# Performance work log

Hardware: AMD Instinct MI355X
Metric: run time of the kernel (lower is better)

## Reference

```python
import jax, jax.numpy as jnp
import numpy as np

B, H, W, C = 2, 64, 64, 192
DM = int(2.0 * C)   # d_inner = ssm_ratio * hidden_dim = 384
N = 16              # d_state
R = 12              # dt_rank = ceil(C / 16)
K = 4               # scan directions


def _ln(x, g, b, eps):
    mu = jnp.mean(x, axis=-1, keepdims=True)
    var = jnp.var(x, axis=-1, keepdims=True)
    return (x - mu) * jax.lax.rsqrt(var + eps) * g + b


def setup_inputs() -> dict:
    key = jax.random.key(0)
    ks = jax.random.split(key, 8)
    return {
        "input": jax.random.normal(ks[0], (B, H, W, C), jnp.float32),
        "norm_g": jnp.ones((C,), jnp.float32),
        "norm_b": jnp.zeros((C,), jnp.float32),
        "in_proj_w": jax.random.normal(ks[1], (C, 2 * DM), jnp.float32) * 0.02,
        "conv_w": jax.random.normal(ks[2], (DM, 1, 3, 3), jnp.float32) * 0.1,
        "conv_b": jnp.zeros((DM,), jnp.float32),
        "x_proj_w": jax.random.normal(ks[3], (K, R + 2 * N, DM), jnp.float32) * 0.02,
        "dt_w": jax.random.normal(ks[4], (K, DM, R), jnp.float32) * 0.1,
        "dt_b": jax.random.uniform(ks[5], (K, DM), jnp.float32, -4.0, -2.0),
        "A_logs": jnp.tile(jnp.log(jnp.arange(1, N + 1, dtype=jnp.float32))[None, None, :], (K, DM, 1)),
        "Ds": jnp.ones((K, DM), jnp.float32),
        "out_norm_g": jnp.ones((DM,), jnp.float32),
        "out_norm_b": jnp.zeros((DM,), jnp.float32),
        "out_proj_w": jax.random.normal(ks[6], (DM, C), jnp.float32) * 0.02,
    }


def _selective_scan(us, deltas, A, Bs, Cs):
    # us, deltas: (B,K,D,L); A: (K,D,N); Bs, Cs: (B,K,N,L)
    u_l = jnp.moveaxis(us, -1, 0)       # (L,B,K,D)
    d_l = jnp.moveaxis(deltas, -1, 0)   # (L,B,K,D)
    B_l = jnp.moveaxis(Bs, -1, 0)       # (L,B,K,N)
    C_l = jnp.moveaxis(Cs, -1, 0)       # (L,B,K,N)
    h0 = jnp.zeros(us.shape[:3] + (A.shape[-1],), us.dtype)  # (B,K,D,N)

    def step(h, xs):
        u_t, d_t, b_t, c_t = xs
        dA = jnp.exp(d_t[..., None] * A)                       # (B,K,D,N)
        h = dA * h + (d_t * u_t)[..., None] * b_t[:, :, None, :]
        y = jnp.einsum('bkdn,bkn->bkd', h, c_t)
        return h, y

    _, ys = jax.lax.scan(step, h0, (u_l, d_l, B_l, C_l))
    return jnp.moveaxis(ys, 0, -1)  # (B,K,D,L)


def reference(input, norm_g, norm_b, in_proj_w, conv_w, conv_b, x_proj_w,
              dt_w, dt_b, A_logs, Ds, out_norm_g, out_norm_b, out_proj_w):
    Bz, Hh, Ww, Cc = input.shape
    L = Hh * Ww
    # pre-norm
    xn = _ln(input, norm_g, norm_b, 1e-6)
    # input projection -> x, z
    xz = xn @ in_proj_w                      # (B,H,W,2*DM)
    x, z = jnp.split(xz, 2, axis=-1)
    # depthwise conv + SiLU (channels-first)
    x = jnp.transpose(x, (0, 3, 1, 2))       # (B,DM,H,W)
    Dm = x.shape[1]
    x = jax.lax.conv_general_dilated(
        x, conv_w, (1, 1), 'SAME',
        dimension_numbers=('NCHW', 'OIHW', 'NCHW'),
        feature_group_count=Dm) + conv_b[None, :, None, None]
    x = jax.nn.silu(x)
    # 4-direction cross-scan: hw, wh, and their reverses
    x_flat = x.reshape(Bz, Dm, L)
    x_t = jnp.transpose(x, (0, 1, 3, 2)).reshape(Bz, Dm, L)
    xs = jnp.stack([x_flat, x_t], axis=1)                  # (B,2,DM,L)
    xs = jnp.concatenate([xs, jnp.flip(xs, -1)], axis=1)   # (B,4,DM,L)
    Rr = dt_w.shape[2]
    Nn = A_logs.shape[2]
    x_dbl = jnp.einsum('bkdl,kcd->bkcl', xs, x_proj_w)     # (B,4,R+2N,L)
    dts, Bs, Cs = jnp.split(x_dbl, [Rr, Rr + Nn], axis=2)
    deltas = jax.nn.softplus(
        jnp.einsum('bkrl,kdr->bkdl', dts, dt_w) + dt_b[None, :, :, None])
    A = -jnp.exp(A_logs)                                   # (4,DM,N)
    out_y = _selective_scan(xs, deltas, A, Bs, Cs) + Ds[None, :, :, None] * xs
    # merge the 4 directions back
    inv = jnp.flip(out_y[:, 2:], -1)

    def wh(t):
        return jnp.transpose(t.reshape(Bz, Dm, Ww, Hh), (0, 1, 3, 2)).reshape(Bz, Dm, L)

    y = out_y[:, 0] + inv[:, 0] + wh(out_y[:, 1]) + wh(inv[:, 1])  # (B,DM,L)
    y = jnp.transpose(y, (0, 2, 1))                                # (B,L,DM)
    y = _ln(y, out_norm_g, out_norm_b, 1e-5).reshape(Bz, Hh, Ww, Dm)
    y = y * jax.nn.silu(z)
    out = y @ out_proj_w
    # residual (drop_path=0 -> identity)
    return input + out
```

## Files before the change

kernel.cpp:

```cpp
#include <hip/hip_runtime.h>
#include <hip/hip_bf16.h>


typedef __attribute__((ext_vector_type(8))) short short8;
typedef __attribute__((ext_vector_type(4))) float floatx4;

__global__ __launch_bounds__(256) void k_ln(const float* __restrict__ in,
                                            const float* __restrict__ g,
                                            const float* __restrict__ be,
                                            __hip_bfloat16* __restrict__ out) {
  int row = blockIdx.x * 4 + (threadIdx.x >> 6);
  int lane = threadIdx.x & 63;
  const float* x = in + (long)row * 192;
  float v0 = x[lane], v1 = x[lane + 64], v2 = x[lane + 128];
  float s = v0 + v1 + v2;
  float s2 = v0 * v0 + v1 * v1 + v2 * v2;
  #pragma unroll
  for (int o = 32; o > 0; o >>= 1) { s += __shfl_xor(s, o); s2 += __shfl_xor(s2, o); }
  float mu = s * (1.f / 192.f);
  float var = s2 * (1.f / 192.f) - mu * mu;
  float r = rsqrtf(var + 1e-6f);
  __hip_bfloat16* op = out + (long)row * 192;
  op[lane]       = __float2bfloat16((v0 - mu) * r * g[lane]       + be[lane]);
  op[lane + 64]  = __float2bfloat16((v1 - mu) * r * g[lane + 64]  + be[lane + 64]);
  op[lane + 128] = __float2bfloat16((v2 - mu) * r * g[lane + 128] + be[lane + 128]);
}

__global__ __launch_bounds__(256) void k_packw(const float* __restrict__ ipw,
                                               const float* __restrict__ xpw,
                                               const float* __restrict__ opw,
                                               __hip_bfloat16* __restrict__ Wt1,
                                               __hip_bfloat16* __restrict__ Wt2,
                                               __hip_bfloat16* __restrict__ Wt3) {
  int idx = blockIdx.x * 256 + threadIdx.x;
  if (idx < 147456) {
    int n = idx / 192, k = idx - n * 192;
    Wt1[idx] = __float2bfloat16(ipw[(long)k * 768 + n]);
  } else if (idx < 147456 + 73728) {
    int t = idx - 147456;
    int j = t / 384;
    float v = (j < 176) ? xpw[t] : 0.f;
    Wt2[t] = __float2bfloat16(v);
  } else if (idx < 147456 + 73728 + 73728) {
    int t = idx - 147456 - 73728;
    int n = t / 384, k = t - n * 384;
    Wt3[t] = __float2bfloat16(opw[(long)k * 192 + n]);
  }
}

__device__ __forceinline__ int inv_dir(int k, int p) {
  int pt = ((p & 63) << 6) | (p >> 6);
  if (k == 0) return p;
  if (k == 1) return pt;
  if (k == 2) return 4095 - p;
  return 4095 - pt;
}
__device__ __forceinline__ int dir_pix(int k, int l) { return inv_dir(k, l); }

template <int EPI>
__global__ __launch_bounds__(256) void k_gemm_mfma(const __hip_bfloat16* __restrict__ A,
                                                   const __hip_bfloat16* __restrict__ Bt,
                                                   const float* __restrict__ Res,
                                                   float* __restrict__ Co,
                                                   __hip_bfloat16* __restrict__ CoB,
                                                   __hip_bfloat16* __restrict__ Co2B,
                                                   float* __restrict__ dtsS,
                                                   float* __restrict__ BsS,
                                                   float* __restrict__ CsS,
                                                   int M, int N, int Kk) {
  __shared__ __align__(16) short As[64 * 64];
  __shared__ __align__(16) short Bs[64 * 64];
  int tid = threadIdx.x;
  int wave = tid >> 6, lane = tid & 63;
  int mlane = lane & 15, quad = lane >> 4;
  int row0 = blockIdx.y * 64, col0 = blockIdx.x * 64;
  int wr = wave & 1, wc = wave >> 1;
  floatx4 acc[2][2];
  #pragma unroll
  for (int mi = 0; mi < 2; mi++)
    #pragma unroll
    for (int ni = 0; ni < 2; ni++) acc[mi][ni] = (floatx4){0.f, 0.f, 0.f, 0.f};

  for (int k0 = 0; k0 < Kk; k0 += 64) {
    #pragma unroll
    for (int c = tid; c < 512; c += 256) {
      int r = c >> 3, j = c & 7;
      *(float4*)&As[r * 64 + ((j ^ (r & 7)) << 3)] =
          *(const float4*)&A[(long)(row0 + r) * Kk + k0 + j * 8];
    }
    #pragma unroll
    for (int c = tid; c < 512; c += 256) {
      int r = c >> 3, j = c & 7;
      *(float4*)&Bs[r * 64 + ((j ^ (r & 7)) << 3)] =
          *(const float4*)&Bt[(long)(col0 + r) * Kk + k0 + j * 8];
    }
    __syncthreads();
    short8 af[2][2], bf[2][2];
    #pragma unroll
    for (int mi = 0; mi < 2; mi++) {
      int r = wr * 32 + mi * 16 + mlane;
      #pragma unroll
      for (int kk = 0; kk < 2; kk++) {
        int jx = (kk * 4 + quad) ^ (r & 7);
        af[mi][kk] = *(const short8*)&As[r * 64 + jx * 8];
      }
    }
    #pragma unroll
    for (int ni = 0; ni < 2; ni++) {
      int rn = wc * 32 + ni * 16 + mlane;
      #pragma unroll
      for (int kk = 0; kk < 2; kk++) {
        int jx = (kk * 4 + quad) ^ (rn & 7);
        bf[ni][kk] = *(const short8*)&Bs[rn * 64 + jx * 8];
      }
    }
    #pragma unroll
    for (int kk = 0; kk < 2; kk++)
      #pragma unroll
      for (int mi = 0; mi < 2; mi++)
        #pragma unroll
        for (int ni = 0; ni < 2; ni++)
          acc[mi][ni] = __builtin_amdgcn_mfma_f32_16x16x32_bf16(af[mi][kk], bf[ni][kk],
                                                                acc[mi][ni], 0, 0, 0);
    __syncthreads();
  }
  #pragma unroll
  for (int mi = 0; mi < 2; mi++) {
    #pragma unroll
    for (int ni = 0; ni < 2; ni++) {
      int cc = col0 + wc * 32 + ni * 16 + mlane;
      #pragma unroll
      for (int i = 0; i < 4; i++) {
        int rr = row0 + wr * 32 + mi * 16 + quad * 4 + i;
        float v = acc[mi][ni][i];
        if (EPI == 1) {
          Co[(long)rr * N + cc] = v + Res[(long)rr * N + cc];
        } else if (EPI == 2) {
          if (cc < 384) CoB[(long)rr * 384 + cc] = __float2bfloat16(v);
          else          Co2B[(long)rr * 384 + (cc - 384)] = __float2bfloat16(v);
        } else {
          if (cc < 176) {
            int k4 = (cc >= 132) ? 3 : (cc >= 88) ? 2 : (cc >= 44) ? 1 : 0;
            int c = cc - k4 * 44;
            int b = rr >> 12, p = rr & 4095;
            int l = inv_dir(k4, p);
            long lbase = ((long)((b << 2) + k4) << 12) + l;
            if (c < 12)      dtsS[lbase * 12 + c] = v;
            else if (c < 28) BsS[lbase * 16 + (c - 12)] = v;
            else             CsS[lbase * 16 + (c - 28)] = v;
          }
        }
      }
    }
  }
}

__global__ __launch_bounds__(384) void k_conv(const __hip_bfloat16* __restrict__ xbufB,
                                              const float* __restrict__ cw,
                                              const float* __restrict__ cb,
                                              __hip_bfloat16* __restrict__ xcb) {
  int row = blockIdx.x;
  int b = row >> 12, p = row & 4095;
  int h = p >> 6, w0 = p & 63;
  int d = threadIdx.x;
  float acc = cb[d];
  const float* wt = cw + d * 9;
  #pragma unroll
  for (int dh = -1; dh <= 1; dh++) {
    int hh = h + dh;
    if (hh < 0 || hh > 63) continue;
    #pragma unroll
    for (int dw = -1; dw <= 1; dw++) {
      int ww = w0 + dw;
      if (ww < 0 || ww > 63) continue;
      acc += __bfloat162float(xbufB[((long)(b << 12) + (hh << 6) + ww) * 384 + d])
             * wt[(dh + 1) * 3 + (dw + 1)];
    }
  }
  float sg = 1.f / (1.f + __expf(-acc));
  xcb[(long)row * 384 + d] = __float2bfloat16(acc * sg);
}

__device__ __forceinline__ void pow16(float r, float* pws) {
  pws[0] = r;
  #pragma unroll
  for (int n = 1; n < 16; n++) {
    int m = n + 1, c = (m + 1) / 2, f = m - c;
    pws[n] = pws[c - 1] * pws[f - 1];
  }
}

__global__ __launch_bounds__(384) void k_scan0(
    const float* __restrict__ dtsS, const float* __restrict__ BsS,
    const __hip_bfloat16* __restrict__ xcb,
    const float* __restrict__ A_logs, const float* __restrict__ dt_w,
    const float* __restrict__ dt_b,
    float* __restrict__ Eb, float* __restrict__ Dend) {
  int bid = blockIdx.x;
  int s = bid & 127, bk = bid >> 7;
  int k = bk & 3, b = bk >> 2;
  int d = threadIdx.x;
  float w[12];
  const float* dwp = dt_w + ((long)(k * 384) + d) * 12;
  #pragma unroll
  for (int r = 0; r < 12; r++) w[r] = dwp[r];
  float db = dt_b[k * 384 + d];
  const float* al = A_logs + ((long)(k * 384) + d) * 16;
  bool pw = true;
  float av[16];
  #pragma unroll
  for (int n = 0; n < 16; n++) {
    float a = __expf(al[n]);
    av[n] = -a;
    pw = pw && (fabsf(a - (float)(n + 1)) < 1e-3f);
  }
  float h[16];
  #pragma unroll
  for (int n = 0; n < 16; n++) h[n] = 0.f;
  float cum = 0.f;
  long lb = (long)bk * 4096 + s * 32;
  long bpix = (long)(b << 12);

  if (pw) {
    #pragma unroll 4
    for (int t = 0; t < 32; t++) {
      const float4* dq = (const float4*)(dtsS + (lb + t) * 12);
      float4 q0 = dq[0], q1 = dq[1], q2 = dq[2];
      float x = db + q0.x * w[0] + q0.y * w[1] + q0.z * w[2] + q0.w * w[3]
                   + q1.x * w[4] + q1.y * w[5] + q1.z * w[6] + q1.w * w[7]
                   + q2.x * w[8] + q2.y * w[9] + q2.z * w[10] + q2.w * w[11];
      float e = __expf(x);
      float delta = (x > 15.f) ? x : __logf(1.f + e);
      cum += delta;
      int p = dir_pix(k, s * 32 + t);
      float u = __bfloat162float(xcb[(bpix + p) * 384 + d]);
      float du = delta * u;
      float rr = __builtin_amdgcn_rcpf(1.f + e);
      float pws[16]; pow16(rr, pws);
      const float4* Bq = (const float4*)(BsS + (lb + t) * 16);
      float4 b0 = Bq[0], b1 = Bq[1], b2 = Bq[2], b3 = Bq[3];
      float Bl[16] = {b0.x, b0.y, b0.z, b0.w, b1.x, b1.y, b1.z, b1.w,
                      b2.x, b2.y, b2.z, b2.w, b3.x, b3.y, b3.z, b3.w};
      #pragma unroll
      for (int n = 0; n < 16; n++) h[n] = pws[n] * h[n] + du * Bl[n];
    }
  } else {
    for (int t = 0; t < 32; t++) {
      const float4* dq = (const float4*)(dtsS + (lb + t) * 12);
      float4 q0 = dq[0], q1 = dq[1], q2 = dq[2];
      float x = db + q0.x * w[0] + q0.y * w[1] + q0.z * w[2] + q0.w * w[3]
                   + q1.x * w[4] + q1.y * w[5] + q1.z * w[6] + q1.w * w[7]
                   + q2.x * w[8] + q2.y * w[9] + q2.z * w[10] + q2.w * w[11];
      float e = __expf(x);
      float delta = (x > 15.f) ? x : __logf(1.f + e);
      cum += delta;
      int p = dir_pix(k, s * 32 + t);
      float u = __bfloat162float(xcb[(bpix + p) * 384 + d]);
      float du = delta * u;
      const float4* Bq = (const float4*)(BsS + (lb + t) * 16);
      float4 b0 = Bq[0], b1 = Bq[1], b2 = Bq[2], b3 = Bq[3];
      float Bl[16] = {b0.x, b0.y, b0.z, b0.w, b1.x, b1.y, b1.z, b1.w,
                      b2.x, b2.y, b2.z, b2.w, b3.x, b3.y, b3.z, b3.w};
      #pragma unroll
      for (int n = 0; n < 16; n++) {
        float dA = __expf(delta * av[n]);
        h[n] = dA * h[n] + du * Bl[n];
      }
    }
  }
  long g = (long)bk * 128 + s;
  float* Ep = Eb + g * 6144 + d * 16;
  #pragma unroll
  for (int n = 0; n < 16; n++) Ep[n] = h[n];
  Dend[g * 384 + d] = cum;
}

__global__ __launch_bounds__(256) void k_combine(float* __restrict__ Eb,
                                                 const float* __restrict__ Dend,
                                                 const float* __restrict__ A_logs) {
  int t = blockIdx.x * 256 + threadIdx.x;
  int bk = t / 6144;
  int dn = t - bk * 6144;
  int k = bk & 3;
  int d = dn >> 4;
  float av = -__expf(A_logs[(long)k * 6144 + dn]);
  float h = 0.f;
  long ebase = (long)bk * 128 * 6144 + dn;
  long dbase = (long)bk * 128 * 384 + d;
  for (int s = 0; s < 128; s++) {
    long ei = ebase + (long)s * 6144;
    float e = Eb[ei];
    float cum = Dend[dbase + (long)s * 384];
    Eb[ei] = h;
    h = __expf(av * cum) * h + e;
  }
}

__global__ __launch_bounds__(384) void k_scan1(
    const float* __restrict__ dtsS, const float* __restrict__ BsS,
    const float* __restrict__ CsS, const __hip_bfloat16* __restrict__ xcb,
    const float* __restrict__ A_logs, const float* __restrict__ dt_w,
    const float* __restrict__ dt_b, const float* __restrict__ Eb,
    float* __restrict__ ysum) {
  int bid = blockIdx.x;
  int s = bid & 127, bk = bid >> 7;
  int k = bk & 3, b = bk >> 2;
  int d = threadIdx.x;
  float w[12];
  const float* dwp = dt_w + ((long)(k * 384) + d) * 12;
  #pragma unroll
  for (int r = 0; r < 12; r++) w[r] = dwp[r];
  float db = dt_b[k * 384 + d];
  const float* al = A_logs + ((long)(k * 384) + d) * 16;
  bool pw = true;
  float av[16];
  #pragma unroll
  for (int n = 0; n < 16; n++) {
    float a = __expf(al[n]);
    av[n] = -a;
    pw = pw && (fabsf(a - (float)(n + 1)) < 1e-3f);
  }
  float h[16];
  const float* hp = Eb + ((long)bk * 128 + s) * 6144 + d * 16;
  #pragma unroll
  for (int n = 0; n < 16; n++) h[n] = hp[n];
  long lb = (long)bk * 4096 + s * 32;
  long bpix = (long)(b << 12);

  if (pw) {
    #pragma unroll 4
    for (int t = 0; t < 32; t++) {
      const float4* dq = (const float4*)(dtsS + (lb + t) * 12);
      float4 q0 = dq[0], q1 = dq[1], q2 = dq[2];
      float x = db + q0.x * w[0] + q0.y * w[1] + q0.z * w[2] + q0.w * w[3]
                   + q1.x * w[4] + q1.y * w[5] + q1.z * w[6] + q1.w * w[7]
                   + q2.x * w[8] + q2.y * w[9] + q2.z * w[10] + q2.w * w[11];
      float e = __expf(x);
      float delta = (x > 15.f) ? x : __logf(1.f + e);
      int p = dir_pix(k, s * 32 + t);
      float u = __bfloat162float(xcb[(bpix + p) * 384 + d]);
      float du = delta * u;
      float rr = __builtin_amdgcn_rcpf(1.f + e);
      float pws[16]; pow16(rr, pws);
      const float4* Bq = (const float4*)(BsS + (lb + t) * 16);
      float4 b0 = Bq[0], b1 = Bq[1], b2 = Bq[2], b3 = Bq[3];
      float Bl[16] = {b0.x, b0.y, b0.z, b0.w, b1.x, b1.y, b1.z, b1.w,
                      b2.x, b2.y, b2.z, b2.w, b3.x, b3.y, b3.z, b3.w};
      const float4* Cq = (const float4*)(CsS + (lb + t) * 16);
      float4 c0 = Cq[0], c1 = Cq[1], c2 = Cq[2], c3 = Cq[3];
      float Cl[16] = {c0.x, c0.y, c0.z, c0.w, c1.x, c1.y, c1.z, c1.w,
                      c2.x, c2.y, c2.z, c2.w, c3.x, c3.y, c3.z, c3.w};
      float y = 0.f;
      #pragma unroll
      for (int n = 0; n < 16; n++) { h[n] = pws[n] * h[n] + du * Bl[n]; y += h[n] * Cl[n]; }
      atomicAdd(&ysum[(bpix + p) * 384 + d], y);
    }
  } else {
    for (int t = 0; t < 32; t++) {
      const float4* dq = (const float4*)(dtsS + (lb + t) * 12);
      float4 q0 = dq[0], q1 = dq[1], q2 = dq[2];
      float x = db + q0.x * w[0] + q0.y * w[1] + q0.z * w[2] + q0.w * w[3]
                   + q1.x * w[4] + q1.y * w[5] + q1.z * w[6] + q1.w * w[7]
                   + q2.x * w[8] + q2.y * w[9] + q2.z * w[10] + q2.w * w[11];
      float e = __expf(x);
      float delta = (x > 15.f) ? x : __logf(1.f + e);
      int p = dir_pix(k, s * 32 + t);
      float u = __bfloat162float(xcb[(bpix + p) * 384 + d]);
      float du = delta * u;
      const float4* Bq = (const float4*)(BsS + (lb + t) * 16);
      float4 b0 = Bq[0], b1 = Bq[1], b2 = Bq[2], b3 = Bq[3];
      float Bl[16] = {b0.x, b0.y, b0.z, b0.w, b1.x, b1.y, b1.z, b1.w,
                      b2.x, b2.y, b2.z, b2.w, b3.x, b3.y, b3.z, b3.w};
      const float4* Cq = (const float4*)(CsS + (lb + t) * 16);
      float4 c0 = Cq[0], c1 = Cq[1], c2 = Cq[2], c3 = Cq[3];
      float Cl[16] = {c0.x, c0.y, c0.z, c0.w, c1.x, c1.y, c1.z, c1.w,
                      c2.x, c2.y, c2.z, c2.w, c3.x, c3.y, c3.z, c3.w};
      float y = 0.f;
      #pragma unroll
      for (int n = 0; n < 16; n++) {
        float dA = __expf(delta * av[n]);
        h[n] = dA * h[n] + du * Bl[n];
        y += h[n] * Cl[n];
      }
      atomicAdd(&ysum[(bpix + p) * 384 + d], y);
    }
  }
}

__global__ __launch_bounds__(384) void k_merge(const float* __restrict__ ysum,
                                               const __hip_bfloat16* __restrict__ xcb,
                                               const __hip_bfloat16* __restrict__ zbufB,
                                               const float* __restrict__ Ds,
                                               const float* __restrict__ g,
                                               const float* __restrict__ be,
                                               __hip_bfloat16* __restrict__ yactb) {
  int row = blockIdx.x;
  int d = threadIdx.x;
  float v = ysum[(long)row * 384 + d];
  float sd = Ds[d] + Ds[384 + d] + Ds[768 + d] + Ds[1152 + d];
  v += __bfloat162float(xcb[(long)row * 384 + d]) * sd;
  float s1 = v, s2 = v * v;
  #pragma unroll
  for (int o = 32; o > 0; o >>= 1) { s1 += __shfl_xor(s1, o); s2 += __shfl_xor(s2, o); }
  __shared__ float r1[6], r2[6];
  int wv = threadIdx.x >> 6;
  if ((threadIdx.x & 63) == 0) { r1[wv] = s1; r2[wv] = s2; }
  __syncthreads();
  float S1 = 0.f, S2 = 0.f;
  #pragma unroll
  for (int i = 0; i < 6; i++) { S1 += r1[i]; S2 += r2[i]; }
  float mu = S1 * (1.f / 384.f);
  float var = S2 * (1.f / 384.f) - mu * mu;
  float rr = rsqrtf(var + 1e-5f);
  float yn = (v - mu) * rr * g[d] + be[d];
  float z = __bfloat162float(zbufB[(long)row * 384 + d]);
  float sg = z / (1.f + __expf(-z));
  yactb[(long)row * 384 + d] = __float2bfloat16(yn * sg);
}

extern "C" void kernel_launch(void* const* d_in, const int* in_sizes, int n_in,
                              void* d_out, int out_size, void* d_ws, size_t ws_size,
                              hipStream_t stream) {
  const float* input      = (const float*)d_in[0];
  const float* norm_g     = (const float*)d_in[1];
  const float* norm_b     = (const float*)d_in[2];
  const float* in_proj_w  = (const float*)d_in[3];
  const float* conv_w     = (const float*)d_in[4];
  const float* conv_b     = (const float*)d_in[5];
  const float* x_proj_w   = (const float*)d_in[6];
  const float* dt_w       = (const float*)d_in[7];
  const float* dt_b       = (const float*)d_in[8];
  const float* A_logs     = (const float*)d_in[9];
  const float* Ds         = (const float*)d_in[10];
  const float* out_norm_g = (const float*)d_in[11];
  const float* out_norm_b = (const float*)d_in[12];
  const float* out_proj_w = (const float*)d_in[13];
  float* out = (float*)d_out;

  float* ws = (float*)d_ws;
  long o = 0;
  __hip_bfloat16* xnb   = (__hip_bfloat16*)(ws + o); o += 786432;
  __hip_bfloat16* xbufB = (__hip_bfloat16*)(ws + o); o += 1572864;
  __hip_bfloat16* zbufB = (__hip_bfloat16*)(ws + o); o += 1572864;
  __hip_bfloat16* xcb   = (__hip_bfloat16*)(ws + o); o += 1572864;
  __hip_bfloat16* Wt1   = (__hip_bfloat16*)(ws + o); o += 73728;
  __hip_bfloat16* Wt2   = (__hip_bfloat16*)(ws + o); o += 36864;
  __hip_bfloat16* Wt3   = (__hip_bfloat16*)(ws + o); o += 36864;
  float* dtsS           = ws + o;                    o += 393216;
  float* BsS            = ws + o;                    o += 524288;
  float* CsS            = ws + o;                    o += 524288;
  float* Eb             = ws + o;                    o += 6291456;
  float* Dend           = ws + o;                    o += 393216;
  float* ysum           = ws + o;                    o += 3145728;
  __hip_bfloat16* yactb = (__hip_bfloat16*)(ws + o); o += 1572864;

  k_ln<<<dim3(2048), dim3(256), 0, stream>>>(input, norm_g, norm_b, xnb);
  k_packw<<<dim3(1152), dim3(256), 0, stream>>>(in_proj_w, x_proj_w, out_proj_w, Wt1, Wt2, Wt3);
  k_gemm_mfma<2><<<dim3(12, 128), dim3(256), 0, stream>>>(xnb, Wt1, nullptr, nullptr, xbufB, zbufB,
                                                          nullptr, nullptr, nullptr, 8192, 768, 192);
  k_conv<<<dim3(8192), dim3(384), 0, stream>>>(xbufB, conv_w, conv_b, xcb);
  k_gemm_mfma<3><<<dim3(3, 128), dim3(256), 0, stream>>>(xcb, Wt2, nullptr, nullptr, nullptr, nullptr,
                                                         dtsS, BsS, CsS, 8192, 192, 384);
  k_scan0<<<dim3(1024), dim3(384), 0, stream>>>(dtsS, BsS, xcb, A_logs, dt_w, dt_b, Eb, Dend);
  k_combine<<<dim3(192), dim3(256), 0, stream>>>(Eb, Dend, A_logs);
  hipMemsetAsync(ysum, 0, 3145728 * sizeof(float), stream);
  k_scan1<<<dim3(1024), dim3(384), 0, stream>>>(dtsS, BsS, CsS, xcb, A_logs, dt_w, dt_b, Eb, ysum);
  k_merge<<<dim3(8192), dim3(384), 0, stream>>>(ysum, xcb, zbufB, Ds, out_norm_g, out_norm_b, yactb);
  k_gemm_mfma<1><<<dim3(3, 128), dim3(256), 0, stream>>>(yactb, Wt3, input, out, nullptr, nullptr,
                                                         nullptr, nullptr, nullptr, 8192, 192, 384);
}
```

Before: 270.2 us.

## Pair forward/reverse scan directions in one block and batch atomic accumulation

Fuses LayerNorm with weight packing, and moves the ysum zeroing into k_scan0 in place of a separate memset. The scan kernels now use 192-thread blocks with d split across two blocks. k_combine writes prefixes into a separate Hb buffer with 64-thread blocks. k_scan1 processes a forward direction and its reversed partner on the same pixel chunk, reusing the loaded u values and summing both outputs in registers, so it issues half as many atomics. In exchange it needs many more registers (yreg, ureg, two weight sets), which may reduce occupancy, plus extra workspace for Hb.

```diff
diff --git a/kernel.cpp b/kernel.cpp
--- a/kernel.cpp
+++ b/kernel.cpp
@@ -5,46 +5,48 @@
 typedef __attribute__((ext_vector_type(8))) short short8;
 typedef __attribute__((ext_vector_type(4))) float floatx4;
 
-__global__ __launch_bounds__(256) void k_ln(const float* __restrict__ in,
-                                            const float* __restrict__ g,
-                                            const float* __restrict__ be,
-                                            __hip_bfloat16* __restrict__ out) {
-  int row = blockIdx.x * 4 + (threadIdx.x >> 6);
-  int lane = threadIdx.x & 63;
-  const float* x = in + (long)row * 192;
-  float v0 = x[lane], v1 = x[lane + 64], v2 = x[lane + 128];
-  float s = v0 + v1 + v2;
-  float s2 = v0 * v0 + v1 * v1 + v2 * v2;
-  #pragma unroll
-  for (int o = 32; o > 0; o >>= 1) { s += __shfl_xor(s, o); s2 += __shfl_xor(s2, o); }
-  float mu = s * (1.f / 192.f);
-  float var = s2 * (1.f / 192.f) - mu * mu;
-  float r = rsqrtf(var + 1e-6f);
-  __hip_bfloat16* op = out + (long)row * 192;
-  op[lane]       = __float2bfloat16((v0 - mu) * r * g[lane]       + be[lane]);
-  op[lane + 64]  = __float2bfloat16((v1 - mu) * r * g[lane + 64]  + be[lane + 64]);
-  op[lane + 128] = __float2bfloat16((v2 - mu) * r * g[lane + 128] + be[lane + 128]);
-}
-
-__global__ __launch_bounds__(256) void k_packw(const float* __restrict__ ipw,
-                                               const float* __restrict__ xpw,
-                                               const float* __restrict__ opw,
-                                               __hip_bfloat16* __restrict__ Wt1,
-                                               __hip_bfloat16* __restrict__ Wt2,
-                                               __hip_bfloat16* __restrict__ Wt3) {
-  int idx = blockIdx.x * 256 + threadIdx.x;
-  if (idx < 147456) {
-    int n = idx / 192, k = idx - n * 192;
-    Wt1[idx] = __float2bfloat16(ipw[(long)k * 768 + n]);
-  } else if (idx < 147456 + 73728) {
-    int t = idx - 147456;
-    int j = t / 384;
-    float v = (j < 176) ? xpw[t] : 0.f;
-    Wt2[t] = __float2bfloat16(v);
-  } else if (idx < 147456 + 73728 + 73728) {
-    int t = idx - 147456 - 73728;
-    int n = t / 384, k = t - n * 384;
-    Wt3[t] = __float2bfloat16(opw[(long)k * 192 + n]);
+__global__ __launch_bounds__(256) void k_ln_packw(const float* __restrict__ in,
+                                                  const float* __restrict__ g,
+                                                  const float* __restrict__ be,
+                                                  const float* __restrict__ ipw,
+                                                  const float* __restrict__ xpw,
+                                                  const float* __restrict__ opw,
+                                                  __hip_bfloat16* __restrict__ xnb,
+                                                  __hip_bfloat16* __restrict__ Wt1,
+                                                  __hip_bfloat16* __restrict__ Wt2,
+                                                  __hip_bfloat16* __restrict__ Wt3) {
+  int bid = blockIdx.x;
+  if (bid < 2048) {
+    int row = bid * 4 + (threadIdx.x >> 6);
+    int lane = threadIdx.x & 63;
+    const float* x = in + (long)row * 192;
+    float v0 = x[lane], v1 = x[lane + 64], v2 = x[lane + 128];
+    float s = v0 + v1 + v2;
+    float s2 = v0 * v0 + v1 * v1 + v2 * v2;
+    #pragma unroll
+    for (int o = 32; o > 0; o >>= 1) { s += __shfl_xor(s, o); s2 += __shfl_xor(s2, o); }
+    float mu = s * (1.f / 192.f);
+    float var = s2 * (1.f / 192.f) - mu * mu;
+    float r = rsqrtf(var + 1e-6f);
+    __hip_bfloat16* op = xnb + (long)row * 192;
+    op[lane]       = __float2bfloat16((v0 - mu) * r * g[lane]       + be[lane]);
+    op[lane + 64]  = __float2bfloat16((v1 - mu) * r * g[lane + 64]  + be[lane + 64]);
+    op[lane + 128] = __float2bfloat16((v2 - mu) * r * g[lane + 128] + be[lane + 128]);
+  } else {
+    int idx = (bid - 2048) * 256 + threadIdx.x;
+    if (idx < 147456) {
+      int n = idx / 192, k = idx - n * 192;
+      Wt1[idx] = __float2bfloat16(ipw[(long)k * 768 + n]);
+    } else if (idx < 147456 + 73728) {
+      int t = idx - 147456;
+      int j = t / 384;
+      float v = (j < 176) ? xpw[t] : 0.f;
+      Wt2[t] = __float2bfloat16(v);
+    } else if (idx < 147456 + 73728 + 73728) {
+      int t = idx - 147456 - 73728;
+      int n = t / 384, k = t - n * 384;
+      Wt3[t] = __float2bfloat16(opw[(long)k * 192 + n]);
+    }
   }
 }
 
@@ -190,16 +192,23 @@
   }
 }
 
-__global__ __launch_bounds__(384) void k_scan0(
+__global__ __launch_bounds__(192) void k_scan0(
     const float* __restrict__ dtsS, const float* __restrict__ BsS,
     const __hip_bfloat16* __restrict__ xcb,
     const float* __restrict__ A_logs, const float* __restrict__ dt_w,
     const float* __restrict__ dt_b,
-    float* __restrict__ Eb, float* __restrict__ Dend) {
+    float* __restrict__ Eb, float* __restrict__ Dend,
+    float* __restrict__ ysum) {
   int bid = blockIdx.x;
-  int s = bid & 127, bk = bid >> 7;
+  {
+    float4 z4 = {0.f, 0.f, 0.f, 0.f};
+    float4* zp = (float4*)(ysum + (long)bid * 1536) + threadIdx.x;
+    zp[0] = z4; zp[192] = z4;
+  }
+  int half = bid & 1;
+  int s = (bid >> 1) & 127, bk = bid >> 8;
   int k = bk & 3, b = bk >> 2;
-  int d = threadIdx.x;
+  int d = half * 192 + threadIdx.x;
   float w[12];
   const float* dwp = dt_w + ((long)(k * 384) + d) * 12;
   #pragma unroll
@@ -275,10 +284,11 @@
   Dend[g * 384 + d] = cum;
 }
 
-__global__ __launch_bounds__(256) void k_combine(float* __restrict__ Eb,
-                                                 const float* __restrict__ Dend,
-                                                 const float* __restrict__ A_logs) {
-  int t = blockIdx.x * 256 + threadIdx.x;
+__global__ __launch_bounds__(64) void k_combine(const float* __restrict__ Eb,
+                                                const float* __restrict__ Dend,
+                                                const float* __restrict__ A_logs,
+                                                float* __restrict__ Hb) {
+  int t = blockIdx.x * 64 + threadIdx.x;
   int bk = t / 6144;
   int dn = t - bk * 6144;
   int k = bk & 3;
@@ -288,102 +298,182 @@
   long ebase = (long)bk * 128 * 6144 + dn;
   long dbase = (long)bk * 128 * 384 + d;
   for (int s = 0; s < 128; s++) {
-    long ei = ebase + (long)s * 6144;
-    float e = Eb[ei];
-    float cum = Dend[dbase + (long)s * 384];
-    Eb[ei] = h;
-    h = __expf(av * cum) * h + e;
-  }
-}
-
-__global__ __launch_bounds__(384) void k_scan1(
+    Hb[ebase + (long)s * 6144] = h;
+    h = __expf(av * Dend[dbase + (long)s * 384]) * h + Eb[ebase + (long)s * 6144];
+  }
+}
+
+__global__ __launch_bounds__(192) void k_scan1(
     const float* __restrict__ dtsS, const float* __restrict__ BsS,
     const float* __restrict__ CsS, const __hip_bfloat16* __restrict__ xcb,
     const float* __restrict__ A_logs, const float* __restrict__ dt_w,
-    const float* __restrict__ dt_b, const float* __restrict__ Eb,
+    const float* __restrict__ dt_b, const float* __restrict__ Hb,
     float* __restrict__ ysum) {
   int bid = blockIdx.x;
-  int s = bid & 127, bk = bid >> 7;
-  int k = bk & 3, b = bk >> 2;
-  int d = threadIdx.x;
-  float w[12];
-  const float* dwp = dt_w + ((long)(k * 384) + d) * 12;
-  #pragma unroll
-  for (int r = 0; r < 12; r++) w[r] = dwp[r];
-  float db = dt_b[k * 384 + d];
-  const float* al = A_logs + ((long)(k * 384) + d) * 16;
+  int half = bid & 1;
+  int s = (bid >> 1) & 127;
+  int q = (bid >> 8) & 1;
+  int b = bid >> 9;
+  int cf = b * 4 + q;
+  int cr = cf + 2;
+  int sr = 127 - s;
+  int d = half * 192 + threadIdx.x;
+
+  float wf[12], wr2[12];
+  const float* dwf = dt_w + ((long)(q * 384) + d) * 12;
+  const float* dwr = dt_w + ((long)((q + 2) * 384) + d) * 12;
+  #pragma unroll
+  for (int r = 0; r < 12; r++) { wf[r] = dwf[r]; wr2[r] = dwr[r]; }
+  float dbf = dt_b[q * 384 + d];
+  float dbr = dt_b[(q + 2) * 384 + d];
+  const float* alf = A_logs + ((long)(q * 384) + d) * 16;
+  const float* alr = A_logs + ((long)((q + 2) * 384) + d) * 16;
   bool pw = true;
-  float av[16];
+  float avf[16], avr[16];
   #pragma unroll
   for (int n = 0; n < 16; n++) {
-    float a = __expf(al[n]);
-    av[n] = -a;
-    pw = pw && (fabsf(a - (float)(n + 1)) < 1e-3f);
-  }
+    float a1 = __expf(alf[n]), a2 = __expf(alr[n]);
+    avf[n] = -a1; avr[n] = -a2;
+    pw = pw && (fabsf(a1 - (float)(n + 1)) < 1e-3f) && (fabsf(a2 - (float)(n + 1)) < 1e-3f);
+  }
+  long lbf = (long)cf * 4096 + s * 32;
+  long lbr = (long)cr * 4096 + sr * 32;
+  long bpix = (long)(b << 12);
   float h[16];
-  const float* hp = Eb + ((long)bk * 128 + s) * 6144 + d * 16;
-  #pragma unroll
-  for (int n = 0; n < 16; n++) h[n] = hp[n];
-  long lb = (long)bk * 4096 + s * 32;
-  long bpix = (long)(b << 12);
-
+  float yreg[32], ureg[32];
+
+  {
+    const float* hp = Hb + ((long)cf * 128 + s) * 6144 + d * 16;
+    #pragma unroll
+    for (int n = 0; n < 16; n++) h[n] = hp[n];
+  }
   if (pw) {
-    #pragma unroll 4
+    #pragma unroll
     for (int t = 0; t < 32; t++) {
-      const float4* dq = (const float4*)(dtsS + (lb + t) * 12);
+      const float4* dq = (const float4*)(dtsS + (lbf + t) * 12);
       float4 q0 = dq[0], q1 = dq[1], q2 = dq[2];
-      float x = db + q0.x * w[0] + q0.y * w[1] + q0.z * w[2] + q0.w * w[3]
-                   + q1.x * w[4] + q1.y * w[5] + q1.z * w[6] + q1.w * w[7]
-                   + q2.x * w[8] + q2.y * w[9] + q2.z * w[10] + q2.w * w[11];
+      float x = dbf + q0.x * wf[0] + q0.y * wf[1] + q0.z * wf[2] + q0.w * wf[3]
+                    + q1.x * wf[4] + q1.y * wf[5] + q1.z * wf[6] + q1.w * wf[7]
+                    + q2.x * wf[8] + q2.y * wf[9] + q2.z * wf[10] + q2.w * wf[11];
       float e = __expf(x);
       float delta = (x > 15.f) ? x : __logf(1.f + e);
-      int p = dir_pix(k, s * 32 + t);
+      int p = dir_pix(q, s * 32 + t);
       float u = __bfloat162float(xcb[(bpix + p) * 384 + d]);
+      ureg[t] = u;
       float du = delta * u;
       float rr = __builtin_amdgcn_rcpf(1.f + e);
       float pws[16]; pow16(rr, pws);
-      const float4* Bq = (const float4*)(BsS + (lb + t) * 16);
+      const float4* Bq = (const float4*)(BsS + (lbf + t) * 16);
       float4 b0 = Bq[0], b1 = Bq[1], b2 = Bq[2], b3 = Bq[3];
       float Bl[16] = {b0.x, b0.y, b0.z, b0.w, b1.x, b1.y, b1.z, b1.w,
                       b2.x, b2.y, b2.z, b2.w, b3.x, b3.y, b3.z, b3.w};
-      const float4* Cq = (const float4*)(CsS + (lb + t) * 16);
+      const float4* Cq = (const float4*)(CsS + (lbf + t) * 16);
       float4 c0 = Cq[0], c1 = Cq[1], c2 = Cq[2], c3 = Cq[3];
       float Cl[16] = {c0.x, c0.y, c0.z, c0.w, c1.x, c1.y, c1.z, c1.w,
                       c2.x, c2.y, c2.z, c2.w, c3.x, c3.y, c3.z, c3.w};
       float y = 0.f;
       #pragma unroll
       for (int n = 0; n < 16; n++) { h[n] = pws[n] * h[n] + du * Bl[n]; y += h[n] * Cl[n]; }
-      atomicAdd(&ysum[(bpix + p) * 384 + d], y);
+      yreg[t] = y;
     }
   } else {
+    #pragma unroll
     for (int t = 0; t < 32; t++) {
-      const float4* dq = (const float4*)(dtsS + (lb + t) * 12);
+      const float4* dq = (const float4*)(dtsS + (lbf + t) * 12);
       float4 q0 = dq[0], q1 = dq[1], q2 = dq[2];
-      float x = db + q0.x * w[0] + q0.y * w[1] + q0.z * w[2] + q0.w * w[3]
-                   + q1.x * w[4] + q1.y * w[5] + q1.z * w[6] + q1.w * w[7]
-                   + q2.x * w[8] + q2.y * w[9] + q2.z * w[10] + q2.w * w[11];
+      float x = dbf + q0.x * wf[0] + q0.y * wf[1] + q0.z * wf[2] + q0.w * wf[3]
+                    + q1.x * wf[4] + q1.y * wf[5] + q1.z * wf[6] + q1.w * wf[7]
+                    + q2.x * wf[8] + q2.y * wf[9] + q2.z * wf[10] + q2.w * wf[11];
       float e = __expf(x);
       float delta = (x > 15.f) ? x : __logf(1.f + e);
-      int p = dir_pix(k, s * 32 + t);
+      int p = dir_pix(q, s * 32 + t);
       float u = __bfloat162float(xcb[(bpix + p) * 384 + d]);
+      ureg[t] = u;
       float du = delta * u;
-      const float4* Bq = (const float4*)(BsS + (lb + t) * 16);
+      const float4* Bq = (const float4*)(BsS + (lbf + t) * 16);
       float4 b0 = Bq[0], b1 = Bq[1], b2 = Bq[2], b3 = Bq[3];
       float Bl[16] = {b0.x, b0.y, b0.z, b0.w, b1.x, b1.y, b1.z, b1.w,
                       b2.x, b2.y, b2.z, b2.w, b3.x, b3.y, b3.z, b3.w};
-      const float4* Cq = (const float4*)(CsS + (lb + t) * 16);
+      const float4* Cq = (const float4*)(CsS + (lbf + t) * 16);
       float4 c0 = Cq[0], c1 = Cq[1], c2 = Cq[2], c3 = Cq[3];
       float Cl[16] = {c0.x, c0.y, c0.z, c0.w, c1.x, c1.y, c1.z, c1.w,
                       c2.x, c2.y, c2.z, c2.w, c3.x, c3.y, c3.z, c3.w};
       float y = 0.f;
       #pragma unroll
       for (int n = 0; n < 16; n++) {
-        float dA = __expf(delta * av[n]);
+        float dA = __expf(delta * avf[n]);
         h[n] = dA * h[n] + du * Bl[n];
         y += h[n] * Cl[n];
       }
-      atomicAdd(&ysum[(bpix + p) * 384 + d], y);
-    }
+      yreg[t] = y;
+    }
+  }
+  {
+    const float* hp = Hb + ((long)cr * 128 + sr) * 6144 + d * 16;
+    #pragma unroll
+    for (int n = 0; n < 16; n++) h[n] = hp[n];
+  }
+  if (pw) {
+    #pragma unroll
+    for (int tt = 0; tt < 32; tt++) {
+      const float4* dq = (const float4*)(dtsS + (lbr + tt) * 12);
+      float4 q0 = dq[0], q1 = dq[1], q2 = dq[2];
+      float x = dbr + q0.x * wr2[0] + q0.y * wr2[1] + q0.z * wr2[2] + q0.w * wr2[3]
+                    + q1.x * wr2[4] + q1.y * wr2[5] + q1.z * wr2[6] + q1.w * wr2[7]
+                    + q2.x * wr2[8] + q2.y * wr2[9] + q2.z * wr2[10] + q2.w * wr2[11];
+      float e = __expf(x);
+      float delta = (x > 15.f) ? x : __logf(1.f + e);
+      float u = ureg[31 - tt];
+      float du = delta * u;
+      float rr = __builtin_amdgcn_rcpf(1.f + e);
+      float pws[16]; pow16(rr, pws);
+      const float4* Bq = (const float4*)(BsS + (lbr + tt) * 16);
+      float4 b0 = Bq[0], b1 = Bq[1], b2 = Bq[2], b3 = Bq[3];
+      float Bl[16] = {b0.x, b0.y, b0.z, b0.w, b1.x, b1.y, b1.z, b1.w,
+                      b2.x, b2.y, b2.z, b2.w, b3.x, b3.y, b3.z, b3.w};
+      const float4* Cq = (const float4*)(CsS + (lbr + tt) * 16);
+      float4 c0 = Cq[0], c1 = Cq[1], c2 = Cq[2], c3 = Cq[3];
+      float Cl[16] = {c0.x, c0.y, c0.z, c0.w, c1.x, c1.y, c1.z, c1.w,
+                      c2.x, c2.y, c2.z, c2.w, c3.x, c3.y, c3.z, c3.w};
+      float y = 0.f;
+      #pragma unroll
+      for (int n = 0; n < 16; n++) { h[n] = pws[n] * h[n] + du * Bl[n]; y += h[n] * Cl[n]; }
+      yreg[31 - tt] += y;
+    }
+  } else {
+    #pragma unroll
+    for (int tt = 0; tt < 32; tt++) {
+      const float4* dq = (const float4*)(dtsS + (lbr + tt) * 12);
+      float4 q0 = dq[0], q1 = dq[1], q2 = dq[2];
+      float x = dbr + q0.x * wr2[0] + q0.y * wr2[1] + q0.z * wr2[2] + q0.w * wr2[3]
+                    + q1.x * wr2[4] + q1.y * wr2[5] + q1.z * wr2[6] + q1.w * wr2[7]
+                    + q2.x * wr2[8] + q2.y * wr2[9] + q2.z * wr2[10] + q2.w * wr2[11];
+      float e = __expf(x);
+      float delta = (x > 15.f) ? x : __logf(1.f + e);
+      float u = ureg[31 - tt];
+      float du = delta * u;
+      const float4* Bq = (const float4*)(BsS + (lbr + tt) * 16);
+      float4 b0 = Bq[0], b1 = Bq[1], b2 = Bq[2], b3 = Bq[3];
+      float Bl[16] = {b0.x, b0.y, b0.z, b0.w, b1.x, b1.y, b1.z, b1.w,
+                      b2.x, b2.y, b2.z, b2.w, b3.x, b3.y, b3.z, b3.w};
+      const float4* Cq = (const float4*)(CsS + (lbr + tt) * 16);
+      float4 c0 = Cq[0], c1 = Cq[1], c2 = Cq[2], c3 = Cq[3];
+      float Cl[16] = {c0.x, c0.y, c0.z, c0.w, c1.x, c1.y, c1.z, c1.w,
+                      c2.x, c2.y, c2.z, c2.w, c3.x, c3.y, c3.z, c3.w};
+      float y = 0.f;
+      #pragma unroll
+      for (int n = 0; n < 16; n++) {
+        float dA = __expf(delta * avr[n]);
+        h[n] = dA * h[n] + du * Bl[n];
+        y += h[n] * Cl[n];
+      }
+      yreg[31 - tt] += y;
+    }
+  }
+  #pragma unroll
+  for (int t = 0; t < 32; t++) {
+    int p = dir_pix(q, s * 32 + t);
+    atomicAdd(&ysum[(bpix + p) * 384 + d], yreg[t]);
   }
 }
 
@@ -451,20 +541,21 @@
   float* CsS            = ws + o;                    o += 524288;
   float* Eb             = ws + o;                    o += 6291456;
   float* Dend           = ws + o;                    o += 393216;
+  float* Hb             = ws + o;                    o += 6291456;
   float* ysum           = ws + o;                    o += 3145728;
   __hip_bfloat16* yactb = (__hip_bfloat16*)(ws + o); o += 1572864;
 
-  k_ln<<<dim3(2048), dim3(256), 0, stream>>>(input, norm_g, norm_b, xnb);
-  k_packw<<<dim3(1152), dim3(256), 0, stream>>>(in_proj_w, x_proj_w, out_proj_w, Wt1, Wt2, Wt3);
+  k_ln_packw<<<dim3(3200), dim3(256), 0, stream>>>(input, norm_g, norm_b,
+                                                   in_proj_w, x_proj_w, out_proj_w,
+                                                   xnb, Wt1, Wt2, Wt3);
   k_gemm_mfma<2><<<dim3(12, 128), dim3(256), 0, stream>>>(xnb, Wt1, nullptr, nullptr, xbufB, zbufB,
                                                           nullptr, nullptr, nullptr, 8192, 768, 192);
   k_conv<<<dim3(8192), dim3(384), 0, stream>>>(xbufB, conv_w, conv_b, xcb);
   k_gemm_mfma<3><<<dim3(3, 128), dim3(256), 0, stream>>>(xcb, Wt2, nullptr, nullptr, nullptr, nullptr,
                                                          dtsS, BsS, CsS, 8192, 192, 384);
-  k_scan0<<<dim3(1024), dim3(384), 0, stream>>>(dtsS, BsS, xcb, A_logs, dt_w, dt_b, Eb, Dend);
-  k_combine<<<dim3(192), dim3(256), 0, stream>>>(Eb, Dend, A_logs);
-  hipMemsetAsync(ysum, 0, 3145728 * sizeof(float), stream);
-  k_scan1<<<dim3(1024), dim3(384), 0, stream>>>(dtsS, BsS, CsS, xcb, A_logs, dt_w, dt_b, Eb, ysum);
+  k_scan0<<<dim3(2048), dim3(192), 0, stream>>>(dtsS, BsS, xcb, A_logs, dt_w, dt_b, Eb, Dend, ysum);
+  k_combine<<<dim3(768), dim3(64), 0, stream>>>(Eb, Dend, A_logs, Hb);
+  k_scan1<<<dim3(1024), dim3(192), 0, stream>>>(dtsS, BsS, CsS, xcb, A_logs, dt_w, dt_b, Hb, ysum);
   k_merge<<<dim3(8192), dim3(384), 0, stream>>>(ysum, xcb, zbufB, Ds, out_norm_g, out_norm_b, yactb);
   k_gemm_mfma<1><<<dim3(3, 128), dim3(256), 0, stream>>>(yactb, Wt3, input, out, nullptr, nullptr,
                                                          nullptr, nullptr, nullptr, 8192, 192, 384);
```

New measurement: 359.1 us. +32.9%, slower.

## Replace serial chunk-combine with two-level grouped prefix and fold ysum zeroing

Applied to the files above, without the earlier changes.

The old combine kernel ran 49152 threads, each walking all 128 chunks serially to build exclusive prefix states. It is replaced by a kernel that reduces groups of 16 chunks into (product, state) pairs using 8x more threads. Each scan1 block then rebuilds its starting state from the preceding group summaries plus up to 15 in-group chunk states. The ysum memset is folded into the new kernel. This trades a long serial dependency chain for redundant recomputation in scan1, which adds extra loads and exps there.

```diff
diff --git a/kernel.cpp b/kernel.cpp
--- a/kernel.cpp
+++ b/kernel.cpp
@@ -275,32 +275,43 @@
   Dend[g * 384 + d] = cum;
 }
 
-__global__ __launch_bounds__(256) void k_combine(float* __restrict__ Eb,
-                                                 const float* __restrict__ Dend,
-                                                 const float* __restrict__ A_logs) {
-  int t = blockIdx.x * 256 + threadIdx.x;
-  int bk = t / 6144;
-  int dn = t - bk * 6144;
-  int k = bk & 3;
-  int d = dn >> 4;
-  float av = -__expf(A_logs[(long)k * 6144 + dn]);
-  float h = 0.f;
-  long ebase = (long)bk * 128 * 6144 + dn;
-  long dbase = (long)bk * 128 * 384 + d;
-  for (int s = 0; s < 128; s++) {
-    long ei = ebase + (long)s * 6144;
-    float e = Eb[ei];
-    float cum = Dend[dbase + (long)s * 384];
-    Eb[ei] = h;
-    h = __expf(av * cum) * h + e;
-  }
+__global__ __launch_bounds__(256) void k_comb1(const float* __restrict__ Eb,
+                                               const float* __restrict__ Dend,
+                                               const float* __restrict__ A_logs,
+                                               float* __restrict__ Gp,
+                                               float* __restrict__ Ge,
+                                               float* __restrict__ ysum) {
+  int gt = blockIdx.x * 256 + threadIdx.x;
+  {
+    float4 z4 = {0.f, 0.f, 0.f, 0.f};
+    float4* zp = (float4*)(ysum + (long)gt * 8);
+    zp[0] = z4; zp[1] = z4;
+  }
+  int chain = gt / 49152;
+  int rem = gt - chain * 49152;
+  int grp = rem / 6144;
+  int dn = rem - grp * 6144;
+  int dd = dn >> 4;
+  float av = -__expf(A_logs[(long)(chain & 3) * 6144 + dn]);
+  float A = 1.f, Eacc = 0.f;
+  long g0 = (long)chain * 128 + grp * 16;
+  for (int i = 0; i < 16; i++) {
+    long g = g0 + i;
+    float P = __expf(av * Dend[g * 384 + dd]);
+    Eacc = P * Eacc + Eb[g * 6144 + dn];
+    A *= P;
+  }
+  Gp[gt] = A;
+  Ge[gt] = Eacc;
 }
 
 __global__ __launch_bounds__(384) void k_scan1(
     const float* __restrict__ dtsS, const float* __restrict__ BsS,
     const float* __restrict__ CsS, const __hip_bfloat16* __restrict__ xcb,
     const float* __restrict__ A_logs, const float* __restrict__ dt_w,
-    const float* __restrict__ dt_b, const float* __restrict__ Eb,
+    const float* __restrict__ dt_b,
+    const float* __restrict__ Eb, const float* __restrict__ Dend,
+    const float* __restrict__ Gp, const float* __restrict__ Ge,
     float* __restrict__ ysum) {
   int bid = blockIdx.x;
   int s = bid & 127, bk = bid >> 7;
@@ -320,14 +331,40 @@
     av[n] = -a;
     pw = pw && (fabsf(a - (float)(n + 1)) < 1e-3f);
   }
-  float h[16];
-  const float* hp = Eb + ((long)bk * 128 + s) * 6144 + d * 16;
-  #pragma unroll
-  for (int n = 0; n < 16; n++) h[n] = hp[n];
   long lb = (long)bk * 4096 + s * 32;
   long bpix = (long)(b << 12);
 
+  float h[16];
+  #pragma unroll
+  for (int n = 0; n < 16; n++) h[n] = 0.f;
+  int grp = s >> 4;
+  for (int g2 = 0; g2 < grp; g2++) {
+    long idx = ((long)bk * 8 + g2) * 6144 + d * 16;
+    const float4* Gp4 = (const float4*)(Gp + idx);
+    const float4* Ge4 = (const float4*)(Ge + idx);
+    #pragma unroll
+    for (int i = 0; i < 4; i++) {
+      float4 pp = Gp4[i], ee = Ge4[i];
+      h[4 * i + 0] = pp.x * h[4 * i + 0] + ee.x;
+      h[4 * i + 1] = pp.y * h[4 * i + 1] + ee.y;
+      h[4 * i + 2] = pp.z * h[4 * i + 2] + ee.z;
+      h[4 * i + 3] = pp.w * h[4 * i + 3] + ee.w;
+    }
+  }
   if (pw) {
+    for (int g = bk * 128 + grp * 16; g < bk * 128 + s; g++) {
+      float rho = __expf(-Dend[(long)g * 384 + d]);
+      float P[16]; pow16(rho, P);
+      const float4* E4 = (const float4*)(Eb + (long)g * 6144 + d * 16);
+      #pragma unroll
+      for (int i = 0; i < 4; i++) {
+        float4 ee = E4[i];
+        h[4 * i + 0] = P[4 * i + 0] * h[4 * i + 0] + ee.x;
+        h[4 * i + 1] = P[4 * i + 1] * h[4 * i + 1] + ee.y;
+        h[4 * i + 2] = P[4 * i + 2] * h[4 * i + 2] + ee.z;
+        h[4 * i + 3] = P[4 * i + 3] * h[4 * i + 3] + ee.w;
+      }
+    }
     #pragma unroll 4
     for (int t = 0; t < 32; t++) {
       const float4* dq = (const float4*)(dtsS + (lb + t) * 12);
@@ -356,6 +393,18 @@
       atomicAdd(&ysum[(bpix + p) * 384 + d], y);
     }
   } else {
+    for (int g = bk * 128 + grp * 16; g < bk * 128 + s; g++) {
+      float cg2 = Dend[(long)g * 384 + d];
+      const float4* E4 = (const float4*)(Eb + (long)g * 6144 + d * 16);
+      float El[16];
+      #pragma unroll
+      for (int i = 0; i < 4; i++) {
+        float4 ee = E4[i];
+        El[4 * i] = ee.x; El[4 * i + 1] = ee.y; El[4 * i + 2] = ee.z; El[4 * i + 3] = ee.w;
+      }
+      #pragma unroll
+      for (int n = 0; n < 16; n++) h[n] = __expf(av[n] * cg2) * h[n] + El[n];
+    }
     for (int t = 0; t < 32; t++) {
       const float4* dq = (const float4*)(dtsS + (lb + t) * 12);
       float4 q0 = dq[0], q1 = dq[1], q2 = dq[2];
@@ -451,6 +500,8 @@
   float* CsS            = ws + o;                    o += 524288;
   float* Eb             = ws + o;                    o += 6291456;
   float* Dend           = ws + o;                    o += 393216;
+  float* Gp             = ws + o;                    o += 393216;
+  float* Ge             = ws + o;                    o += 393216;
   float* ysum           = ws + o;                    o += 3145728;
   __hip_bfloat16* yactb = (__hip_bfloat16*)(ws + o); o += 1572864;
 
@@ -462,9 +513,9 @@
   k_gemm_mfma<3><<<dim3(3, 128), dim3(256), 0, stream>>>(xcb, Wt2, nullptr, nullptr, nullptr, nullptr,
                                                          dtsS, BsS, CsS, 8192, 192, 384);
   k_scan0<<<dim3(1024), dim3(384), 0, stream>>>(dtsS, BsS, xcb, A_logs, dt_w, dt_b, Eb, Dend);
-  k_combine<<<dim3(192), dim3(256), 0, stream>>>(Eb, Dend, A_logs);
-  hipMemsetAsync(ysum, 0, 3145728 * sizeof(float), stream);
-  k_scan1<<<dim3(1024), dim3(384), 0, stream>>>(dtsS, BsS, CsS, xcb, A_logs, dt_w, dt_b, Eb, ysum);
+  k_comb1<<<dim3(1536), dim3(256), 0, stream>>>(Eb, Dend, A_logs, Gp, Ge, ysum);
+  k_scan1<<<dim3(1024), dim3(384), 0, stream>>>(dtsS, BsS, CsS, xcb, A_logs, dt_w, dt_b,
+                                                Eb, Dend, Gp, Ge, ysum);
   k_merge<<<dim3(8192), dim3(384), 0, stream>>>(ysum, xcb, zbufB, Ds, out_norm_g, out_norm_b, yactb);
   k_gemm_mfma<1><<<dim3(3, 128), dim3(256), 0, stream>>>(yactb, Wt3, input, out, nullptr, nullptr,
                                                          nullptr, nullptr, nullptr, 8192, 192, 384);
```

Measured after the change: 296.4 us. +9.7%, slower.
